# Kernel tuning notes

Hardware: AMD Instinct MI355X
Metric: run time of the kernel (lower is better)

The kernel has to match this reference:

```python
import jax, jax.numpy as jnp
import numpy as np

B, T, D, H = 8, 1024, 512, 8
CH = D // H          # chunk_size = d_model // num_heads
PAD = 0              # pad_token_id
MAX_TRANS = 1024     # translen cap from source
NINF = float('-inf')


def setup_inputs() -> dict:
    key = jax.random.key(0)
    ks = jax.random.split(key, 8)
    features = jax.random.normal(ks[0], (B, T, D), jnp.float32)
    pos_embed = jax.random.normal(ks[1], (B, T, D), jnp.float32)
    tokens = jax.random.randint(ks[2], (B, T), 0, 32000, dtype=jnp.int32)
    Wq = jax.random.normal(ks[3], (D, 2 * D), jnp.float32) * 0.02
    bq = jnp.zeros((D,), jnp.float32)
    Wk = jax.random.normal(ks[4], (D, 2 * D), jnp.float32) * 0.02
    bk = jnp.zeros((D,), jnp.float32)
    Wg = jax.random.normal(ks[5], (H, 2 * D), jnp.float32) * 0.02
    bg = jnp.zeros((H,), jnp.float32)
    return dict(features=features, pos_embed=pos_embed, tokens=tokens,
                Wq=Wq, bq=bq, Wk=Wk, bk=bk, Wg=Wg, bg=bg)


def _safe_log_softmax(x, axis):
    # matches torch F.log_softmax followed by re-masking: rows that are all -inf stay -inf
    m = jnp.max(x, axis=axis, keepdims=True)
    allinf = jnp.isneginf(m)
    m_safe = jnp.where(allinf, 0.0, m)
    lse = m_safe + jnp.log(jnp.sum(jnp.exp(x - m_safe), axis=axis, keepdims=True))
    lse = jnp.where(allinf, 0.0, lse)
    return x - lse


def _safe_logsumexp(x, axis):
    # matches the custom logsumexp helper in the source (all -inf -> -inf, no nan)
    m = jnp.max(x, axis=axis)
    mask = jnp.isneginf(m)
    m_safe = jnp.where(mask, 0.0, m)
    s = jnp.sum(jnp.exp(x - jnp.expand_dims(m_safe, axis)), axis=axis)
    return jnp.log(jnp.where(mask, 1.0, s)) + jnp.where(mask, NINF, m_safe)


def reference(features, pos_embed, tokens, Wq, bq, Wk, bk, Wg, bg):
    # features_withpos = cat(decoder_out, link positional embedding)  -> [B, T, 2D]
    f = jnp.concatenate([features, pos_embed], axis=-1)
    q = (f @ Wq.T + bq).reshape(B, T, H, CH)
    k = (f @ Wk.T + bk).reshape(B, T, H, CH)
    log_gates = jax.nn.log_softmax(f @ Wg.T + bg, axis=-1)  # [B, T, H]
    # einsum 'bicf,bjcf->bijc' with c = head chunk
    scores = jnp.einsum('bihc,bjhc->bijh', q, k) / np.float32(np.sqrt(CH))  # [B,T,T,H]

    translen = min(MAX_TRANS, T - 1)
    n_valid = jnp.sum(tokens != PAD, axis=-1)  # [B]
    # banded indices: position i links to positions i+1 .. i+translen
    band_idx = jnp.arange(T)[:, None] + jnp.arange(translen)[None, :] + 1  # [T, translen]
    invalid = band_idx[None, :, :] >= n_valid[:, None, None]               # [B, T, translen]
    idx_c = jnp.where(invalid, 0, band_idx[None, :, :])
    idx_full = jnp.broadcast_to(idx_c[..., None], (B, T, translen, H))
    extract = jnp.take_along_axis(scores, idx_full, axis=2)                # [B,T,translen,H]
    extract = jnp.where(invalid[..., None], NINF, extract)
    # normalize over transition axis, then mask fully-invalid rows back to -inf
    extract = _safe_log_softmax(extract, axis=2)
    nouse = jnp.all(invalid, axis=-1)                                      # [B, T]
    extract = jnp.where(nouse[:, :, None, None], NINF, extract)
    # head-gated logsumexp over heads -> banded links [B, T, translen]
    links_band = _safe_logsumexp(extract + log_gates[:, :, None, :], axis=-1)
    # restore_valid_links: scatter band back to full [B, T, T] (-inf elsewhere)
    rel = jnp.arange(T)[None, :] - jnp.arange(T)[:, None] - 1              # [T, T]
    valid = (rel >= 0) & (rel < translen)
    rel_c = jnp.clip(rel, 0, translen - 1)
    rel_full = jnp.broadcast_to(rel_c[None, :, :], (B, T, T))
    out = jnp.take_along_axis(links_band, rel_full, axis=2)
    return jnp.where(valid[None, :, :], out, NINF)
```

## Files before the change

kernel.cpp:

```cpp
#include <hip/hip_runtime.h>
#include <math.h>

#define BATCH 8
#define T 1024
#define NH 8
#define NROW 8192
#define NEG_INF (-INFINITY)
#define SENT (-1.0e30f)
#define SC 0.180336880f
#define LOG2E 1.442695041f

typedef __attribute__((ext_vector_type(8))) short short8;
typedef __attribute__((ext_vector_type(4))) float f32x4;

__device__ __forceinline__ ushort f2bf(float x) {
  uint u = __float_as_uint(x);
  return (ushort)((u + 0x7FFFu + ((u >> 16) & 1u)) >> 16);
}
__device__ __forceinline__ uint pack2(float a, float b) {
  return (uint)f2bf(a) | ((uint)f2bf(b) << 16);
}
__device__ __forceinline__ void gl_lds16(const ushort* g, ushort* l) {
  __builtin_amdgcn_global_load_lds(
      (const __attribute__((address_space(1))) unsigned int*)g,
      (__attribute__((address_space(3))) unsigned int*)l, 16, 0, 0);
}

__global__ __launch_bounds__(256) void k_prep(
    const float* __restrict__ feat, const float* __restrict__ pos,
    const int* __restrict__ tokens,
    const float* __restrict__ Wq, const float* __restrict__ Wk,
    const float* __restrict__ Wg, const float* __restrict__ bg,
    ushort* __restrict__ fbf, ushort* __restrict__ Wbf,
    float* __restrict__ gout, int* __restrict__ nvout) {
  const int bid = blockIdx.x;
  const int tid = threadIdx.x;

  if (bid < 1024) {
    __shared__ __align__(16) float Ws[8192];
#pragma unroll
    for (int u = 0; u < 8; ++u)
      ((float4*)Ws)[u * 256 + tid] = ((const float4*)Wg)[u * 256 + tid];
    __syncthreads();

    const int w = tid >> 6, l = tid & 63;
    const int c0 = l * 16;
    const int row0 = bid * 8 + w * 2;

    float4 f[2][4];
#pragma unroll
    for (int r = 0; r < 2; ++r) {
      const int row = row0 + r;
      const float* src = (c0 < 512) ? (feat + (size_t)row * 512 + c0)
                                    : (pos + (size_t)row * 512 + (c0 - 512));
#pragma unroll
      for (int q4 = 0; q4 < 4; ++q4) f[r][q4] = *(const float4*)(src + q4 * 4);
      uint4 o0, o1;
      o0.x = pack2(f[r][0].x, f[r][0].y); o0.y = pack2(f[r][0].z, f[r][0].w);
      o0.z = pack2(f[r][1].x, f[r][1].y); o0.w = pack2(f[r][1].z, f[r][1].w);
      o1.x = pack2(f[r][2].x, f[r][2].y); o1.y = pack2(f[r][2].z, f[r][2].w);
      o1.z = pack2(f[r][3].x, f[r][3].y); o1.w = pack2(f[r][3].z, f[r][3].w);
      *(uint4*)(fbf + (size_t)row * 1024 + c0) = o0;
      *(uint4*)(fbf + (size_t)row * 1024 + c0 + 8) = o1;
    }

    float s[2][8];
#pragma unroll
    for (int h = 0; h < 8; ++h) {
      const float* wg = Ws + h * 1024 + c0;
      float4 w0 = *(const float4*)(wg + 0);
      float4 w1 = *(const float4*)(wg + 4);
      float4 w2 = *(const float4*)(wg + 8);
      float4 w3 = *(const float4*)(wg + 12);
#pragma unroll
      for (int r = 0; r < 2; ++r)
        s[r][h] = f[r][0].x * w0.x + f[r][0].y * w0.y + f[r][0].z * w0.z + f[r][0].w * w0.w
                + f[r][1].x * w1.x + f[r][1].y * w1.y + f[r][1].z * w1.z + f[r][1].w * w1.w
                + f[r][2].x * w2.x + f[r][2].y * w2.y + f[r][2].z * w2.z + f[r][2].w * w2.w
                + f[r][3].x * w3.x + f[r][3].y * w3.y + f[r][3].z * w3.z + f[r][3].w * w3.w;
    }
#pragma unroll
    for (int m = 1; m < 64; m <<= 1)
#pragma unroll
      for (int r = 0; r < 2; ++r)
#pragma unroll
        for (int h = 0; h < 8; ++h) s[r][h] += __shfl_xor(s[r][h], m, 64);
    if (l == 0) {
#pragma unroll
      for (int r = 0; r < 2; ++r) {
        float lg[8], mx = -1e30f;
#pragma unroll
        for (int h = 0; h < 8; ++h) { lg[h] = s[r][h] + bg[h]; mx = fmaxf(mx, lg[h]); }
        float sum = 0.f;
#pragma unroll
        for (int h = 0; h < 8; ++h) sum += __expf(lg[h] - mx);
        const float lse = mx + __logf(sum);
#pragma unroll
        for (int h = 0; h < 8; ++h) gout[(size_t)(row0 + r) * 8 + h] = lg[h] - lse;
      }
    }
  } else if (bid < 1536) {
    const int gid = (bid - 1024) * 256 + tid;
    const int e0 = gid * 8;
    const int n = e0 >> 10, k = e0 & 1023;
    const float* src = (n < 512) ? (Wq + (size_t)n * 1024 + k)
                                 : (Wk + (size_t)(n - 512) * 1024 + k);
    float4 a = *(const float4*)src;
    float4 b = *(const float4*)(src + 4);
    uint4 o;
    o.x = pack2(a.x, a.y); o.y = pack2(a.z, a.w);
    o.z = pack2(b.x, b.y); o.w = pack2(b.z, b.w);
    *(uint4*)(Wbf + (size_t)n * 1024 + k) = o;
  } else {
    const int b = bid - 1536;
    int cnt = 0;
    for (int i = tid; i < T; i += 256) cnt += (tokens[b * T + i] != 0) ? 1 : 0;
    __shared__ int s[256];
    s[tid] = cnt;
    __syncthreads();
    for (int st = 128; st > 0; st >>= 1) {
      if (tid < st) s[tid] += s[tid + st];
      __syncthreads();
    }
    if (tid == 0) nvout[b] = s[0];
  }
}

__global__ __launch_bounds__(256) void k_gemm(
    const ushort* __restrict__ fbf, const ushort* __restrict__ Wbf,
    const float* __restrict__ bq, const float* __restrict__ bk,
    ushort* __restrict__ qbuf, ushort* __restrict__ kbuf) {
  const int g = blockIdx.x + 8 * blockIdx.y;
  const int wid = (g & 7) * 64 + (g >> 3);
  const int n0 = (wid & 7) * 128;
  const int m0 = (wid >> 3) * 128;
  const int tid = threadIdx.x;
  const int w = tid >> 6, l = tid & 63;
  const int lo = l & 15, quad = l >> 4;
  const int wm0 = (w >> 1) * 64, wn0 = (w & 1) * 64;

  __shared__ ushort As[2][128 * 64];
  __shared__ ushort Bs[2][128 * 64];

  f32x4 acc[4][4];
#pragma unroll
  for (int i = 0; i < 4; ++i)
#pragma unroll
    for (int j = 0; j < 4; ++j) acc[i][j] = (f32x4){0.f, 0.f, 0.f, 0.f};

  const int c8 = (tid & 7) * 8;
  const int r0 = tid >> 3;

  auto stage = [&](int buf, int k0) {
#pragma unroll
    for (int u = 0; u < 4; ++u) {
      gl_lds16(fbf + (size_t)(m0 + u * 32 + r0) * 1024 + k0 + c8,
               As[buf] + (size_t)w * 512 + u * 2048);
      gl_lds16(Wbf + (size_t)(n0 + u * 32 + r0) * 1024 + k0 + c8,
               Bs[buf] + (size_t)w * 512 + u * 2048);
    }
  };

  stage(0, 0);
  int cur = 0;
  for (int k0 = 0; k0 < 1024; k0 += 64) {
    __syncthreads();
    if (k0 + 64 < 1024) stage(cur ^ 1, k0 + 64);
    const ushort* pA = As[cur];
    const ushort* pB = Bs[cur];
#pragma unroll
    for (int kk = 0; kk < 2; ++kk) {
      short8 af[4], bfr[4];
#pragma unroll
      for (int mi = 0; mi < 4; ++mi)
        af[mi] = *(const short8*)(pA + (size_t)(wm0 + mi * 16 + lo) * 64 + kk * 32 + quad * 8);
#pragma unroll
      for (int ni = 0; ni < 4; ++ni)
        bfr[ni] = *(const short8*)(pB + (size_t)(wn0 + ni * 16 + lo) * 64 + kk * 32 + quad * 8);
#pragma unroll
      for (int mi = 0; mi < 4; ++mi)
#pragma unroll
        for (int ni = 0; ni < 4; ++ni)
          acc[mi][ni] = __builtin_amdgcn_mfma_f32_16x16x32_bf16(bfr[ni], af[mi], acc[mi][ni], 0, 0, 0);
    }
    cur ^= 1;
  }

  float4 bias4[4];
#pragma unroll
  for (int ni = 0; ni < 4; ++ni) {
    const int gn = n0 + wn0 + ni * 16 + quad * 4;
    bias4[ni] = *(const float4*)((gn < 512) ? (bq + gn) : (bk + gn - 512));
  }
#pragma unroll
  for (int mi = 0; mi < 4; ++mi) {
    const int m = m0 + wm0 + mi * 16 + lo;
#pragma unroll
    for (int ni = 0; ni < 4; ++ni) {
      const int gn = n0 + wn0 + ni * 16 + quad * 4;
      ushort* dst = (gn < 512) ? (qbuf + (size_t)m * 512 + gn)
                               : (kbuf + (size_t)m * 512 + gn - 512);
      ushort4 o;
      o.x = f2bf(acc[mi][ni][0] + bias4[ni].x);
      o.y = f2bf(acc[mi][ni][1] + bias4[ni].y);
      o.z = f2bf(acc[mi][ni][2] + bias4[ni].z);
      o.w = f2bf(acc[mi][ni][3] + bias4[ni].w);
      *(ushort4*)dst = o;
    }
  }
}

__global__ __launch_bounds__(256) void k_pass1(
    const ushort* __restrict__ q, const ushort* __restrict__ kv,
    const float* __restrict__ g, const int* __restrict__ nvp,
    float* __restrict__ Wt) {
  const int it = blockIdx.x, h = blockIdx.y, b = blockIdx.z;
  const int nv = nvp[b];
  const int i0 = it * 64;
  const int tid = threadIdx.x;
  const int w = tid >> 6, l = tid & 63;
  const int lo = l & 15, quad = l >> 4;

  __shared__ ushort Ks[2][64 * 64];

  const int i = i0 + w * 16 + lo;
  const ushort* qp = q + (size_t)(b * T + i) * 512 + h * 64 + quad * 8;
  const short8 a0 = *(const short8*)qp;
  const short8 a1 = *(const short8*)(qp + 32);

  float lsum = 0.f;
  const int ntile = ((nv + 63) >> 6) - it;

  if (ntile > 0) {
    auto stage = [&](int buf, int jt) {
#pragma unroll
      for (int u = 0; u < 2; ++u) {
        const int s = u * 256 + tid;
        const int row = s >> 3, c = s & 7;
        gl_lds16(kv + (size_t)(b * T + jt * 64 + row) * 512 + h * 64 + ((c ^ (row & 7)) * 8),
                 Ks[buf] + (size_t)(u * 256 + w * 64) * 8);
      }
    };
    stage(0, it);
    __syncthreads();
    for (int s = 0; s < ntile; ++s) {
      if (s + 1 < ntile) stage((s + 1) & 1, it + s + 1);
      const ushort* kbase = Ks[s & 1];
      const int j0 = (it + s) * 64;
      const bool diag = (s == 0);
      const bool masked = diag | (j0 + 64 > nv);
#pragma unroll
      for (int ni = 0; ni < 4; ++ni) {
        if (diag && ni < w) continue;
        const int rw = ni * 16 + lo;
        const short8 b0 = *(const short8*)(kbase + (size_t)rw * 64 + ((quad ^ (rw & 7)) * 8));
        const short8 b1 = *(const short8*)(kbase + (size_t)rw * 64 + (((4 + quad) ^ (rw & 7)) * 8));
        f32x4 acc = (f32x4){0.f, 0.f, 0.f, 0.f};
        acc = __builtin_amdgcn_mfma_f32_16x16x32_bf16(b0, a0, acc, 0, 0, 0);
        acc = __builtin_amdgcn_mfma_f32_16x16x32_bf16(b1, a1, acc, 0, 0, 0);
        if (!masked) {
#pragma unroll
          for (int r = 0; r < 4; ++r) lsum += __builtin_amdgcn_exp2f(acc[r] * SC);
        } else {
          const int jb = j0 + ni * 16 + quad * 4;
#pragma unroll
          for (int r = 0; r < 4; ++r) {
            const int j = jb + r;
            if (j > i && j < nv) lsum += __builtin_amdgcn_exp2f(acc[r] * SC);
          }
        }
      }
      __syncthreads();
    }
  }

  lsum += __shfl_xor(lsum, 16, 64);
  lsum += __shfl_xor(lsum, 32, 64);
  if (quad == 0) {
    const size_t row = (size_t)(b * T) + i;
    Wt[(size_t)h * NROW + row] =
        (lsum > 0.f) ? (g[row * 8 + h] - __logf(lsum)) : NEG_INF;
  }
}

__global__ __launch_bounds__(256) void k_pass2(
    const ushort* __restrict__ q, const ushort* __restrict__ kv,
    const float* __restrict__ Wt, const int* __restrict__ nvp,
    float* __restrict__ out) {
  const int jt = blockIdx.x, it = blockIdx.y, b = blockIdx.z;
  const int nv = nvp[b];
  const int i0 = it * 64, j0 = jt * 64;
  const int tid = threadIdx.x;

  if (jt < it || j0 >= nv) {
    const int r0 = tid >> 4, c0 = (tid & 15) * 4;
    float4 v; v.x = v.y = v.z = v.w = SENT;
#pragma unroll
    for (int u = 0; u < 4; ++u)
      *(float4*)(out + ((size_t)(b * T + i0 + r0 + u * 16)) * T + j0 + c0) = v;
    return;
  }

  const int w = tid >> 6, l = tid & 63;
  const int lo = l & 15, quad = l >> 4;
  const int i = i0 + w * 16 + lo;

  __shared__ ushort Ks[2][64 * 64];

  auto stage = [&](int buf, int h) {
#pragma unroll
    for (int u = 0; u < 2; ++u) {
      const int s = u * 256 + tid;
      const int row = s >> 3, c = s & 7;
      gl_lds16(kv + (size_t)(b * T + j0 + row) * 512 + h * 64 + ((c ^ (row & 7)) * 8),
               Ks[buf] + (size_t)(u * 256 + w * 64) * 8);
    }
  };

  stage(0, 0);

  const ushort* qb = q + (size_t)(b * T + i) * 512 + quad * 8;
  short8 qa0[8], qa1[8];
  float wl[8];
#pragma unroll
  for (int h = 0; h < 8; ++h) {
    qa0[h] = *(const short8*)(qb + h * 64);
    qa1[h] = *(const short8*)(qb + h * 64 + 32);
    wl[h] = Wt[(size_t)h * NROW + b * T + i] * LOG2E;
  }

  float se[4][4];
#pragma unroll
  for (int a = 0; a < 4; ++a)
#pragma unroll
    for (int c = 0; c < 4; ++c) se[a][c] = 0.f;

  __syncthreads();

#pragma unroll
  for (int h = 0; h < 8; ++h) {
    if (h < 7) stage((h + 1) & 1, h + 1);
    const ushort* kbase = Ks[h & 1];
#pragma unroll
    for (int ni = 0; ni < 4; ++ni) {
      const int rw = ni * 16 + lo;
      const short8 b0 = *(const short8*)(kbase + (size_t)rw * 64 + ((quad ^ (rw & 7)) * 8));
      const short8 b1 = *(const short8*)(kbase + (size_t)rw * 64 + (((4 + quad) ^ (rw & 7)) * 8));
      f32x4 acc = (f32x4){0.f, 0.f, 0.f, 0.f};
      acc = __builtin_amdgcn_mfma_f32_16x16x32_bf16(b0, qa0[h], acc, 0, 0, 0);
      acc = __builtin_amdgcn_mfma_f32_16x16x32_bf16(b1, qa1[h], acc, 0, 0, 0);
#pragma unroll
      for (int r = 0; r < 4; ++r)
        se[ni][r] += __builtin_amdgcn_exp2f(acc[r] * SC + wl[h]);
    }
    if (h < 7) __syncthreads();
  }

  const size_t orow = ((size_t)(b * T + i)) * T;
#pragma unroll
  for (int ni = 0; ni < 4; ++ni) {
    const int jb = j0 + ni * 16 + quad * 4;
    float4 v;
    v.x = (jb + 0 > i && jb + 0 < nv) ? fmaxf(__logf(se[ni][0]), SENT) : SENT;
    v.y = (jb + 1 > i && jb + 1 < nv) ? fmaxf(__logf(se[ni][1]), SENT) : SENT;
    v.z = (jb + 2 > i && jb + 2 < nv) ? fmaxf(__logf(se[ni][2]), SENT) : SENT;
    v.w = (jb + 3 > i && jb + 3 < nv) ? fmaxf(__logf(se[ni][3]), SENT) : SENT;
    *(float4*)(out + orow + jb) = v;
  }
}

extern "C" void kernel_launch(void* const* d_in, const int* in_sizes, int n_in,
                              void* d_out, int out_size, void* d_ws, size_t ws_size,
                              hipStream_t stream) {
  (void)in_sizes; (void)n_in; (void)out_size; (void)ws_size;
  const float* feat = (const float*)d_in[0];
  const float* pos  = (const float*)d_in[1];
  const int* tokens = (const int*)d_in[2];
  const float* Wq = (const float*)d_in[3];
  const float* bq = (const float*)d_in[4];
  const float* Wk = (const float*)d_in[5];
  const float* bk = (const float*)d_in[6];
  const float* Wg = (const float*)d_in[7];
  const float* bg = (const float*)d_in[8];
  float* out = (float*)d_out;

  ushort* qbuf = (ushort*)d_ws;
  ushort* kbuf = qbuf + (size_t)NROW * 512;
  ushort* Wbf  = kbuf + (size_t)NROW * 512;
  float*  gbuf = (float*)(Wbf + (size_t)1024 * 1024);
  float*  Wt   = gbuf + (size_t)NROW * NH;
  int*    nv   = (int*)(Wt + (size_t)NH * NROW);

  ushort* fbf = (ushort*)d_out;

  k_prep<<<dim3(1544), dim3(256), 0, stream>>>(feat, pos, tokens, Wq, Wk, Wg, bg,
                                               fbf, Wbf, gbuf, nv);
  k_gemm<<<dim3(8, 64), dim3(256), 0, stream>>>(fbf, Wbf, bq, bk, qbuf, kbuf);
  k_pass1<<<dim3(16, NH, BATCH), dim3(256), 0, stream>>>(qbuf, kbuf, gbuf, nv, Wt);
  k_pass2<<<dim3(16, 16, BATCH), dim3(256), 0, stream>>>(qbuf, kbuf, Wt, nv, out);
}
```

Baseline: 182.5 us.

## Enlarge pass2 tiles to 128x128 with LDS-staged Q and reorder grid dims

Pass2 now processes 128x128 output tiles with 512 threads and 8 waves, each wave computing a 32x64 sub-tile. Q is staged through LDS alongside K (double-buffered per head), so each K and Q fragment is reused across more MFMAs. The block indices of both passes are reordered so that batch is the fastest-varying grid dimension. This is meant to raise compute per byte loaded and spread causal work more evenly across the blocks in flight, at the cost of more LDS per block, lower occupancy, and more wasted work on diagonal tiles.

```diff
diff --git a/kernel.cpp b/kernel.cpp
--- a/kernel.cpp
+++ b/kernel.cpp
@@ -214,7 +214,7 @@
     const ushort* __restrict__ q, const ushort* __restrict__ kv,
     const float* __restrict__ g, const int* __restrict__ nvp,
     float* __restrict__ Wt) {
-  const int it = blockIdx.x, h = blockIdx.y, b = blockIdx.z;
+  const int b = blockIdx.x, h = blockIdx.y, it = blockIdx.z;
   const int nv = nvp[b];
   const int i0 = it * 64;
   const int tid = threadIdx.x;
@@ -283,89 +283,114 @@
   }
 }
 
-__global__ __launch_bounds__(256) void k_pass2(
+__global__ __launch_bounds__(512) void k_pass2(
     const ushort* __restrict__ q, const ushort* __restrict__ kv,
     const float* __restrict__ Wt, const int* __restrict__ nvp,
     float* __restrict__ out) {
-  const int jt = blockIdx.x, it = blockIdx.y, b = blockIdx.z;
+  const int b = blockIdx.x, jt = blockIdx.y, it = blockIdx.z;
   const int nv = nvp[b];
-  const int i0 = it * 64, j0 = jt * 64;
+  const int i0 = it * 128, j0 = jt * 128;
   const int tid = threadIdx.x;
 
   if (jt < it || j0 >= nv) {
-    const int r0 = tid >> 4, c0 = (tid & 15) * 4;
+    const int r0 = tid >> 5, c0 = (tid & 31) * 4;
     float4 v; v.x = v.y = v.z = v.w = SENT;
 #pragma unroll
-    for (int u = 0; u < 4; ++u)
+    for (int u = 0; u < 8; ++u)
       *(float4*)(out + ((size_t)(b * T + i0 + r0 + u * 16)) * T + j0 + c0) = v;
     return;
   }
 
   const int w = tid >> 6, l = tid & 63;
   const int lo = l & 15, quad = l >> 4;
-  const int i = i0 + w * 16 + lo;
-
-  __shared__ ushort Ks[2][64 * 64];
+  const int qi = w & 3, qj = w >> 2;
+
+  __shared__ ushort Qs[2][128 * 64];
+  __shared__ ushort Ks[2][128 * 64];
 
   auto stage = [&](int buf, int h) {
 #pragma unroll
     for (int u = 0; u < 2; ++u) {
-      const int s = u * 256 + tid;
+      const int s = u * 512 + tid;
       const int row = s >> 3, c = s & 7;
+      gl_lds16(q  + (size_t)(b * T + i0 + row) * 512 + h * 64 + ((c ^ (row & 7)) * 8),
+               Qs[buf] + (size_t)(u * 512 + w * 64) * 8);
       gl_lds16(kv + (size_t)(b * T + j0 + row) * 512 + h * 64 + ((c ^ (row & 7)) * 8),
-               Ks[buf] + (size_t)(u * 256 + w * 64) * 8);
+               Ks[buf] + (size_t)(u * 512 + w * 64) * 8);
     }
   };
 
   stage(0, 0);
 
-  const ushort* qb = q + (size_t)(b * T + i) * 512 + quad * 8;
-  short8 qa0[8], qa1[8];
-  float wl[8];
-#pragma unroll
-  for (int h = 0; h < 8; ++h) {
-    qa0[h] = *(const short8*)(qb + h * 64);
-    qa1[h] = *(const short8*)(qb + h * 64 + 32);
-    wl[h] = Wt[(size_t)h * NROW + b * T + i] * LOG2E;
-  }
-
-  float se[4][4];
-#pragma unroll
-  for (int a = 0; a < 4; ++a)
-#pragma unroll
-    for (int c = 0; c < 4; ++c) se[a][c] = 0.f;
+  float wl[2][8];
+#pragma unroll
+  for (int mi = 0; mi < 2; ++mi) {
+    const int i = i0 + qi * 32 + mi * 16 + lo;
+#pragma unroll
+    for (int h = 0; h < 8; ++h)
+      wl[mi][h] = Wt[(size_t)h * NROW + b * T + i] * LOG2E;
+  }
+
+  float se[2][4][4];
+#pragma unroll
+  for (int a = 0; a < 2; ++a)
+#pragma unroll
+    for (int c = 0; c < 4; ++c)
+#pragma unroll
+      for (int r = 0; r < 4; ++r) se[a][c][r] = 0.f;
 
   __syncthreads();
 
 #pragma unroll
   for (int h = 0; h < 8; ++h) {
     if (h < 7) stage((h + 1) & 1, h + 1);
-    const ushort* kbase = Ks[h & 1];
+    const ushort* Qb = Qs[h & 1];
+    const ushort* Kb = Ks[h & 1];
+    f32x4 acc[2][4];
+#pragma unroll
+    for (int mi = 0; mi < 2; ++mi)
+#pragma unroll
+      for (int ni = 0; ni < 4; ++ni) acc[mi][ni] = (f32x4){0.f, 0.f, 0.f, 0.f};
+#pragma unroll
+    for (int kk = 0; kk < 2; ++kk) {
+      const int swz = ((kk * 4 + quad) ^ (lo & 7)) * 8;
+      short8 qf[2], kf[4];
+#pragma unroll
+      for (int mi = 0; mi < 2; ++mi)
+        qf[mi] = *(const short8*)(Qb + (size_t)(qi * 32 + mi * 16 + lo) * 64 + swz);
+#pragma unroll
+      for (int ni = 0; ni < 4; ++ni)
+        kf[ni] = *(const short8*)(Kb + (size_t)(qj * 64 + ni * 16 + lo) * 64 + swz);
+#pragma unroll
+      for (int mi = 0; mi < 2; ++mi)
+#pragma unroll
+        for (int ni = 0; ni < 4; ++ni)
+          acc[mi][ni] = __builtin_amdgcn_mfma_f32_16x16x32_bf16(kf[ni], qf[mi], acc[mi][ni], 0, 0, 0);
+    }
+#pragma unroll
+    for (int mi = 0; mi < 2; ++mi)
+#pragma unroll
+      for (int ni = 0; ni < 4; ++ni)
+#pragma unroll
+        for (int r = 0; r < 4; ++r)
+          se[mi][ni][r] += __builtin_amdgcn_exp2f(acc[mi][ni][r] * SC + wl[mi][h]);
+    if (h < 7) __syncthreads();
+  }
+
+#pragma unroll
+  for (int mi = 0; mi < 2; ++mi) {
+    const int i = i0 + qi * 32 + mi * 16 + lo;
+    const size_t orow = ((size_t)(b * T + i)) * T;
 #pragma unroll
     for (int ni = 0; ni < 4; ++ni) {
-      const int rw = ni * 16 + lo;
-      const short8 b0 = *(const short8*)(kbase + (size_t)rw * 64 + ((quad ^ (rw & 7)) * 8));
-      const short8 b1 = *(const short8*)(kbase + (size_t)rw * 64 + (((4 + quad) ^ (rw & 7)) * 8));
-      f32x4 acc = (f32x4){0.f, 0.f, 0.f, 0.f};
-      acc = __builtin_amdgcn_mfma_f32_16x16x32_bf16(b0, qa0[h], acc, 0, 0, 0);
-      acc = __builtin_amdgcn_mfma_f32_16x16x32_bf16(b1, qa1[h], acc, 0, 0, 0);
-#pragma unroll
-      for (int r = 0; r < 4; ++r)
-        se[ni][r] += __builtin_amdgcn_exp2f(acc[r] * SC + wl[h]);
-    }
-    if (h < 7) __syncthreads();
-  }
-
-  const size_t orow = ((size_t)(b * T + i)) * T;
-#pragma unroll
-  for (int ni = 0; ni < 4; ++ni) {
-    const int jb = j0 + ni * 16 + quad * 4;
-    float4 v;
-    v.x = (jb + 0 > i && jb + 0 < nv) ? fmaxf(__logf(se[ni][0]), SENT) : SENT;
-    v.y = (jb + 1 > i && jb + 1 < nv) ? fmaxf(__logf(se[ni][1]), SENT) : SENT;
-    v.z = (jb + 2 > i && jb + 2 < nv) ? fmaxf(__logf(se[ni][2]), SENT) : SENT;
-    v.w = (jb + 3 > i && jb + 3 < nv) ? fmaxf(__logf(se[ni][3]), SENT) : SENT;
-    *(float4*)(out + orow + jb) = v;
+      const int jb = j0 + qj * 64 + ni * 16 + quad * 4;
+      float4 v;
+      v.x = (jb + 0 > i && jb + 0 < nv) ? fmaxf(__logf(se[mi][ni][0]), SENT) : SENT;
+      v.y = (jb + 1 > i && jb + 1 < nv) ? fmaxf(__logf(se[mi][ni][1]), SENT) : SENT;
+      v.z = (jb + 2 > i && jb + 2 < nv) ? fmaxf(__logf(se[mi][ni][2]), SENT) : SENT;
+      v.w = (jb + 3 > i && jb + 3 < nv) ? fmaxf(__logf(se[mi][ni][3]), SENT) : SENT;
+      *(float4*)(out + orow + jb) = v;
+    }
   }
 }
 
@@ -396,6 +421,6 @@
   k_prep<<<dim3(1544), dim3(256), 0, stream>>>(feat, pos, tokens, Wq, Wk, Wg, bg,
                                                fbf, Wbf, gbuf, nv);
   k_gemm<<<dim3(8, 64), dim3(256), 0, stream>>>(fbf, Wbf, bq, bk, qbuf, kbuf);
-  k_pass1<<<dim3(16, NH, BATCH), dim3(256), 0, stream>>>(qbuf, kbuf, gbuf, nv, Wt);
-  k_pass2<<<dim3(16, 16, BATCH), dim3(256), 0, stream>>>(qbuf, kbuf, Wt, nv, out);
-}
+  k_pass1<<<dim3(BATCH, NH, 16), dim3(256), 0, stream>>>(qbuf, kbuf, gbuf, nv, Wt);
+  k_pass2<<<dim3(BATCH, 8, 8), dim3(512), 0, stream>>>(qbuf, kbuf, Wt, nv, out);
+}
```

Result: faster. 165.8 us (-9.1%).
